# Performance work log

Measured on AMD Instinct MI355X. Metric: run time of the kernel, lower is better.

The kernel has to match this reference:

```python
import jax, jax.numpy as jnp
import numpy as np

N_NODES = 50000
N_EDGES = 800000
IN_CH = 256
HID = 64
OUT_CH = 64
N_LAYERS = 3
ALPHA = 0.1


def _gpr_temp():
    t = ALPHA * (1.0 - ALPHA) ** np.arange(N_LAYERS + 1)
    t[-1] = (1.0 - ALPHA) ** N_LAYERS
    return jnp.asarray(t, dtype=jnp.float32)


def setup_inputs() -> dict:
    key = jax.random.key(0)
    ks = jax.random.split(key, 8)
    x = jax.random.normal(ks[0], (N_NODES, IN_CH), dtype=jnp.float32)
    edge_index = jax.random.randint(ks[1], (2, N_EDGES), 0, N_NODES, dtype=jnp.int64 if jax.config.jax_enable_x64 else jnp.int32).astype(jnp.int32)
    edge_w = jax.random.uniform(ks[2], (N_EDGES,), dtype=jnp.float32)
    # xavier-uniform-ish scales
    W_in = jax.random.normal(ks[3], (IN_CH, HID), dtype=jnp.float32) * (1.0 / np.sqrt(IN_CH))
    b_in = jnp.zeros((HID,), dtype=jnp.float32)
    layer_W = jax.random.normal(ks[4], (N_LAYERS, HID, HID), dtype=jnp.float32) * (1.0 / np.sqrt(HID))
    layer_b = jnp.zeros((N_LAYERS, HID), dtype=jnp.float32)
    W_out = jax.random.normal(ks[5], (HID, OUT_CH), dtype=jnp.float32) * (1.0 / np.sqrt(HID))
    b_out = jnp.zeros((OUT_CH,), dtype=jnp.float32)
    temp = _gpr_temp()
    return {"x": x, "edge_index": edge_index, "edge_w": edge_w, "W_in": W_in,
            "b_in": b_in, "layer_W": layer_W, "layer_b": layer_b,
            "W_out": W_out, "b_out": b_out, "temp": temp}


def reference(x, edge_index, edge_w, W_in, b_in, layer_W, layer_b, W_out, b_out, temp):
    src, dst = edge_index[0], edge_index[1]
    # inlinear
    h = x @ W_in + b_in                      # [N, HID]
    # GPR combination: hidden = sum_k temp[k] * relu(SpMM(linear(h_k)))
    hidden = h * temp[0]
    cur = h
    for i in range(layer_W.shape[0]):
        z = cur @ layer_W[i] + layer_b[i]    # [N, HID]
        m = z[src] * edge_w[:, None]         # gather + edge weight, [E, HID]
        agg = jax.ops.segment_sum(m, dst, num_segments=x.shape[0])  # scatter-sum
        cur = jax.nn.relu(agg)               # dropout is identity in eval mode
        hidden = hidden + cur * temp[i + 1]
    return hidden @ W_out + b_out            # [N, OUT_CH]
```

## Files before the change

### kernel.cpp

```cpp
#include <hip/hip_runtime.h>
#include <hip/hip_bf16.h>

#define NN 50000
#define NE 800000
#define CIN 256
#define HH 64
#define NBINS 196
#define B1 256
#define EPB 3125
#define NGB 782
#define NLB 3125

typedef unsigned long long u64;
typedef __attribute__((ext_vector_type(8))) short short8;
typedef __attribute__((ext_vector_type(4))) float f32x4;

__device__ __forceinline__ float bf2f(ushort u) {
    union { unsigned int i; float f; } v; v.i = ((unsigned int)u) << 16; return v.f;
}
__device__ __forceinline__ ushort f2bf(float f) {
    __hip_bfloat16 b = __float2bfloat16(f);
    return *reinterpret_cast<ushort*>(&b);
}

__global__ __launch_bounds__(256) void k_prep(
    const float* __restrict__ W_in, const float* __restrict__ LW,
    const float* __restrict__ W_out, ushort* __restrict__ Wp)
{
    const int tid = blockIdx.x * 256 + threadIdx.x;
    if (tid < 16384) {
        const int i = tid & 7;
        const int l = (tid >> 3) & 63;
        const int s = (tid >> 9) & 7;
        const int t = tid >> 12;
        const int k = s * 32 + (l >> 4) * 8 + i;
        const int c = t * 16 + (l & 15);
        Wp[tid] = f2bf(W_in[k * HH + c]);
    } else {
        const int q = (tid - 16384) & 4095;
        const int m = (tid - 16384) >> 12;
        const int i = q & 7;
        const int l = (q >> 3) & 63;
        const int s = (q >> 9) & 1;
        const int t = q >> 10;
        const int k = s * 32 + (l >> 4) * 8 + i;
        const int c = t * 16 + (l & 15);
        const float* Wm = (m < 3) ? (LW + m * HH * HH) : W_out;
        Wp[tid] = f2bf(Wm[k * HH + c]);
    }
}

__global__ __launch_bounds__(256) void k_fused(
    const float* __restrict__ x, const ushort* __restrict__ Wp,
    const float* __restrict__ b, const int* __restrict__ dst,
    int* __restrict__ H, ushort* __restrict__ h_bf)
{
    __shared__ int hist[NBINS];
    if (blockIdx.x < B1) {
        for (int t = threadIdx.x; t < NBINS; t += 256) hist[t] = 0;
        __syncthreads();
        const int e0 = blockIdx.x * EPB;
        for (int i = threadIdx.x; i < EPB; i += 256)
            atomicAdd(&hist[dst[e0 + i] >> 8], 1);
        __syncthreads();
        for (int t = threadIdx.x; t < NBINS; t += 256)
            H[t * B1 + blockIdx.x] = hist[t];
        return;
    }
    const int w = threadIdx.x >> 6;
    const int l = threadIdx.x & 63;
    const int R0 = (blockIdx.x - B1) * 64 + w * 16;
    const int arow = R0 + (l & 15);
    const int xrow = (arow < NN) ? arow : (NN - 1);
    const float* xr = x + (size_t)xrow * CIN + (l >> 4) * 8;
    const short8* WpV = (const short8*)Wp;

    f32x4 acc0 = {0,0,0,0}, acc1 = {0,0,0,0}, acc2 = {0,0,0,0}, acc3 = {0,0,0,0};
    #pragma unroll
    for (int s = 0; s < 8; ++s) {
        const float4 xa = *(const float4*)(xr + s * 32);
        const float4 xb = *(const float4*)(xr + s * 32 + 4);
        short8 af;
        af[0] = (short)f2bf(xa.x); af[1] = (short)f2bf(xa.y);
        af[2] = (short)f2bf(xa.z); af[3] = (short)f2bf(xa.w);
        af[4] = (short)f2bf(xb.x); af[5] = (short)f2bf(xb.y);
        af[6] = (short)f2bf(xb.z); af[7] = (short)f2bf(xb.w);
        acc0 = __builtin_amdgcn_mfma_f32_16x16x32_bf16(af, WpV[(0*8+s)*64 + l], acc0, 0, 0, 0);
        acc1 = __builtin_amdgcn_mfma_f32_16x16x32_bf16(af, WpV[(1*8+s)*64 + l], acc1, 0, 0, 0);
        acc2 = __builtin_amdgcn_mfma_f32_16x16x32_bf16(af, WpV[(2*8+s)*64 + l], acc2, 0, 0, 0);
        acc3 = __builtin_amdgcn_mfma_f32_16x16x32_bf16(af, WpV[(3*8+s)*64 + l], acc3, 0, 0, 0);
    }
    const int colb = l & 15;
    const int rbase = R0 + (l >> 4) * 4;
    #pragma unroll
    for (int t = 0; t < 4; ++t) {
        const f32x4 a = (t == 0) ? acc0 : (t == 1) ? acc1 : (t == 2) ? acc2 : acc3;
        const float bb = b[t * 16 + colb];
        #pragma unroll
        for (int r = 0; r < 4; ++r) {
            const int row = rbase + r;
            if (row < NN)
                h_bf[(size_t)row * HH + t * 16 + colb] = f2bf(a[r] + bb);
        }
    }
}

__global__ __launch_bounds__(256) void k_scan(
    int* __restrict__ H, int* __restrict__ Sx, int* __restrict__ bcnt)
{
    __shared__ int s[256];
    const int b = blockIdx.x;
    const int t = threadIdx.x;
    int partial = 0;
    for (int idx = t; idx < b * B1; idx += 256) partial += H[idx];
    s[t] = partial;
    __syncthreads();
    #pragma unroll
    for (int off = 128; off > 0; off >>= 1) {
        if (t < off) s[t] += s[t + off];
        __syncthreads();
    }
    const int base = s[0];
    __syncthreads();
    const int v = H[b * B1 + t];
    s[t] = v;
    __syncthreads();
    #pragma unroll
    for (int off = 1; off < 256; off <<= 1) {
        const int add = (t >= off) ? s[t - off] : 0;
        __syncthreads();
        s[t] += add;
        __syncthreads();
    }
    H[b * B1 + t] = s[t] - v + base;
    if (t == 255) { Sx[b] = base; bcnt[b] = s[255]; }
}

__global__ __launch_bounds__(256) void k_scatterA(
    const int* __restrict__ src, const int* __restrict__ dst,
    const float* __restrict__ ew, const int* __restrict__ H,
    int2* __restrict__ tmp_e, ushort* __restrict__ tmp_low)
{
    __shared__ int cur[NBINS];
    for (int t = threadIdx.x; t < NBINS; t += 256)
        cur[t] = H[t * B1 + blockIdx.x];
    __syncthreads();
    const int e0 = blockIdx.x * EPB;
    for (int i = threadIdx.x; i < EPB; i += 256) {
        const int e = e0 + i;
        const int d = dst[e];
        const int pos = atomicAdd(&cur[d >> 8], 1);
        tmp_e[pos] = make_int2(src[e], __float_as_int(ew[e]));
        tmp_low[pos] = (ushort)(d & 255);
    }
}

__global__ __launch_bounds__(512) void k_sortB(
    const int2* __restrict__ tmp_e, const ushort* __restrict__ tmp_low,
    const int* __restrict__ Sx, const int* __restrict__ bcnt,
    int2* __restrict__ epack, int* __restrict__ rowptr, int* __restrict__ cnt)
{
    __shared__ int hist[256], s[256], curs[256];
    const int b = blockIdx.x;
    const int base = Sx[b];
    const int cntE = bcnt[b];
    const int t = threadIdx.x;
    if (t < 256) hist[t] = 0;
    __syncthreads();
    for (int i = t; i < cntE; i += 512)
        atomicAdd(&hist[tmp_low[base + i]], 1);
    __syncthreads();
    if (t < 256) s[t] = hist[t];
    __syncthreads();
    #pragma unroll
    for (int off = 1; off < 256; off <<= 1) {
        const int add = (t < 256 && t >= off) ? s[t - off] : 0;
        __syncthreads();
        if (t < 256) s[t] += add;
        __syncthreads();
    }
    if (t < 256) {
        const int excl = s[t] - hist[t];
        curs[t] = excl;
        const int d = b * 256 + t;
        if (d < NN) { rowptr[d] = base + excl; cnt[d] = hist[t]; }
    }
    __syncthreads();
    for (int i = t; i < cntE; i += 512) {
        const int2 e = tmp_e[base + i];
        const int low = (int)tmp_low[base + i];
        const int pos = base + atomicAdd(&curs[low], 1);
        epack[pos] = e;
    }
}

template<bool FINAL>
__global__ __launch_bounds__(256) void k_layer(
    const ushort* __restrict__ cur_in, ushort* __restrict__ cur_out,
    const int2* __restrict__ epack, const int* __restrict__ rowptr,
    const int* __restrict__ cnt,
    const ushort* __restrict__ WpL, const float* __restrict__ bvec,
    const float* __restrict__ temp,
    const ushort* __restrict__ hbf, const ushort* __restrict__ c1,
    const ushort* __restrict__ WpO, const float* __restrict__ bout,
    float* __restrict__ outp)
{
    __shared__ int2  es[4][64];
    __shared__ ushort ts[16][72];
    __shared__ float swv[16];
    const int w = threadIdx.x >> 6;
    const int j = threadIdx.x & 63;
    const int nb = blockIdx.x * 16;
    const int cg  = j >> 4;
    const int ch4 = j & 15;

    int rsA[4], rcA[4];
    #pragma unroll
    for (int q = 0; q < 4; ++q) {
        rsA[q] = rowptr[nb + w * 4 + q];
        rcA[q] = cnt[nb + w * 4 + q];
    }
    int2 pf = epack[min(rsA[0] + ((j < rcA[0]) ? j : 0), NE - 1)];

    #pragma unroll
    for (int q = 0; q < 4; ++q) {
        const int rs = rsA[q];
        const int rc = rcA[q];
        es[w][j] = pf;
        if (q < 3)
            pf = epack[min(rsA[q+1] + ((j < rcA[q+1]) ? j : 0), NE - 1)];

        float4 acc = {0.0f, 0.0f, 0.0f, 0.0f};
        float  sw  = 0.0f;
        const int m0 = min(rc, 64);
        for (int g = 0; g < m0; g += 16) {
            #pragma unroll
            for (int u = 0; u < 4; ++u) {
                const int idx = g + u * 4 + cg;
                const int sel = (idx < m0) ? idx : 0;
                const int2 p = es[w][sel];
                const float wgt = (idx < m0) ? __int_as_float(p.y) : 0.0f;
                const uint2 v = *(const uint2*)(cur_in + (size_t)p.x * HH + ch4 * 4);
                acc.x = fmaf(wgt, bf2f((ushort)(v.x & 0xffff)), acc.x);
                acc.y = fmaf(wgt, bf2f((ushort)(v.x >> 16)),    acc.y);
                acc.z = fmaf(wgt, bf2f((ushort)(v.y & 0xffff)), acc.z);
                acc.w = fmaf(wgt, bf2f((ushort)(v.y >> 16)),    acc.w);
                sw += wgt;
            }
        }
        for (int base = 64; base < rc; base += 64) {
            const int m = min(rc - base, 64);
            if (j < m) es[w][j] = epack[rs + base + j];
            for (int g = 0; g < m; g += 16) {
                #pragma unroll
                for (int u = 0; u < 4; ++u) {
                    const int idx = g + u * 4 + cg;
                    const int sel = (idx < m) ? idx : 0;
                    const int2 p = es[w][sel];
                    const float wgt = (idx < m) ? __int_as_float(p.y) : 0.0f;
                    const uint2 v = *(const uint2*)(cur_in + (size_t)p.x * HH + ch4 * 4);
                    acc.x = fmaf(wgt, bf2f((ushort)(v.x & 0xffff)), acc.x);
                    acc.y = fmaf(wgt, bf2f((ushort)(v.x >> 16)),    acc.y);
                    acc.z = fmaf(wgt, bf2f((ushort)(v.y & 0xffff)), acc.z);
                    acc.w = fmaf(wgt, bf2f((ushort)(v.y >> 16)),    acc.w);
                    sw += wgt;
                }
            }
        }
        #pragma unroll
        for (int off = 16; off < 64; off <<= 1) {
            acc.x += __shfl_xor(acc.x, off);
            acc.y += __shfl_xor(acc.y, off);
            acc.z += __shfl_xor(acc.z, off);
            acc.w += __shfl_xor(acc.w, off);
            sw    += __shfl_xor(sw, off);
        }
        if (j < 16) {
            const int node = w * 4 + q;
            uint2 o;
            o.x = (uint)f2bf(acc.x) | ((uint)f2bf(acc.y) << 16);
            o.y = (uint)f2bf(acc.z) | ((uint)f2bf(acc.w) << 16);
            *(uint2*)&ts[node][ch4 * 4] = o;
            if (j == 0) swv[node] = sw;
        }
    }
    __syncthreads();

    const int lr = j & 15;
    const int lg = j >> 4;
    const short8 a0 = *(const short8*)&ts[lr][lg * 8];
    const short8 a1 = *(const short8*)&ts[lr][32 + lg * 8];
    if (FINAL) __syncthreads();

    const short8* WpV = (const short8*)WpL;
    f32x4 zac = {0,0,0,0};
    zac = __builtin_amdgcn_mfma_f32_16x16x32_bf16(a0, WpV[(w*2+0)*64 + j], zac, 0, 0, 0);
    zac = __builtin_amdgcn_mfma_f32_16x16x32_bf16(a1, WpV[(w*2+1)*64 + j], zac, 0, 0, 0);

    const float bb = bvec[w * 16 + lr];
    float t0v = 0, t1v = 0, t2v = 0, t3v = 0;
    if (FINAL) { t0v = temp[0]; t1v = temp[1]; t2v = temp[2]; t3v = temp[3]; }
    #pragma unroll
    for (int r = 0; r < 4; ++r) {
        const int row = lg * 4 + r;
        const int n   = nb + row;
        const float z = zac[r] + swv[row] * bb;
        const float rv = fmaxf(z, 0.0f);
        const size_t o = (size_t)n * HH + w * 16 + lr;
        if (!FINAL) {
            cur_out[o] = f2bf(rv);
        } else {
            const float hid = t0v * bf2f(hbf[o]) + t1v * bf2f(c1[o])
                            + t2v * bf2f(cur_in[o]) + t3v * rv;
            ts[row][w * 16 + lr] = f2bf(hid);
        }
    }
    if (FINAL) {
        __syncthreads();
        const short8 b0 = *(const short8*)&ts[lr][lg * 8];
        const short8 b1 = *(const short8*)&ts[lr][32 + lg * 8];
        const short8* WoV = (const short8*)WpO;
        f32x4 oz = {0,0,0,0};
        oz = __builtin_amdgcn_mfma_f32_16x16x32_bf16(b0, WoV[(w*2+0)*64 + j], oz, 0, 0, 0);
        oz = __builtin_amdgcn_mfma_f32_16x16x32_bf16(b1, WoV[(w*2+1)*64 + j], oz, 0, 0, 0);
        const float bo = bout[w * 16 + lr];
        #pragma unroll
        for (int r = 0; r < 4; ++r) {
            const int row = lg * 4 + r;
            outp[(size_t)(nb + row) * HH + w * 16 + lr] = oz[r] + bo;
        }
    }
}

extern "C" void kernel_launch(void* const* d_in, const int* in_sizes, int n_in,
                              void* d_out, int out_size, void* d_ws, size_t ws_size,
                              hipStream_t stream)
{
    const float* x     = (const float*)d_in[0];
    const int*   ei    = (const int*)d_in[1];
    const float* ew    = (const float*)d_in[2];
    const float* W_in  = (const float*)d_in[3];
    const float* b_in  = (const float*)d_in[4];
    const float* LW    = (const float*)d_in[5];
    const float* Lb    = (const float*)d_in[6];
    const float* W_out = (const float*)d_in[7];
    const float* b_out = (const float*)d_in[8];
    const float* temp  = (const float*)d_in[9];
    const int* src = ei;
    const int* dst = ei + NE;

    char* p = (char*)d_ws;
    ushort* h_bf    = (ushort*)p;  p += (size_t)NN * HH * 2;
    ushort* curA    = (ushort*)p;  p += (size_t)NN * HH * 2;
    ushort* curB    = (ushort*)p;  p += (size_t)NN * HH * 2;
    int2*   epack   = (int2*)p;    p += (size_t)NE * 8;
    int2*   tmp_e   = (int2*)p;    p += (size_t)NE * 8;
    ushort* tmp_low = (ushort*)p;  p += (size_t)NE * 2;
    int*    H       = (int*)p;     p += (size_t)NBINS * B1 * 4;
    int*    Sx      = (int*)p;     p += (NBINS + 1) * 4;
    int*    bcnt    = (int*)p;     p += NBINS * 4;
    int*    rowptr  = (int*)p;     p += (size_t)NN * 4;
    int*    cnt     = (int*)p;     p += (size_t)NN * 4;
    ushort* Wp      = (ushort*)p;  p += 32768 * 2;
    float*  out     = (float*)d_out;

    const ushort* WpIn  = Wp;
    const ushort* WpL0  = Wp + 16384;
    const ushort* WpL1  = Wp + 16384 + 4096;
    const ushort* WpL2  = Wp + 16384 + 2 * 4096;
    const ushort* WpOut = Wp + 16384 + 3 * 4096;

    k_prep<<<128, 256, 0, stream>>>(W_in, LW, W_out, Wp);
    k_fused<<<B1 + NGB, 256, 0, stream>>>(x, WpIn, b_in, dst, H, h_bf);
    k_scan<<<NBINS, 256, 0, stream>>>(H, Sx, bcnt);
    k_scatterA<<<B1, 256, 0, stream>>>(src, dst, ew, H, tmp_e, tmp_low);
    k_sortB<<<NBINS, 512, 0, stream>>>(tmp_e, tmp_low, Sx, bcnt, epack, rowptr, cnt);

    k_layer<false><<<NLB, 256, 0, stream>>>(h_bf, curA, epack, rowptr, cnt,
                                            WpL0, Lb + 0 * HH, temp,
                                            nullptr, nullptr, nullptr, nullptr, nullptr);
    k_layer<false><<<NLB, 256, 0, stream>>>(curA, curB, epack, rowptr, cnt,
                                            WpL1, Lb + 1 * HH, temp,
                                            nullptr, nullptr, nullptr, nullptr, nullptr);
    k_layer<true><<<NLB, 256, 0, stream>>>(curB, nullptr, epack, rowptr, cnt,
                                           WpL2, Lb + 2 * HH, temp,
                                           h_bf, curA, WpOut, b_out, out);
}
```

Before: 134.7 us.

## Reorder CSR build stages, pack low dst bits into src, fuse scatter with GEMM

Moves the per-block destination histogram into the weight-prep kernel, runs the scan next, then fuses the first-pass bucket scatter with the input GEMM kernel, cutting one launch. The low 8 bits of dst are packed into the upper half of the src word, which removes the separate tmp_low array and its reads and writes. The GEMM path also preloads all x vectors into registers before the MFMA loop. The packing assumes src fits in 16 bits; node indices up to 49999 do fit, and the high-byte mask in sortB recovers it.

After: 127.4 us (median of 2 runs). 1.06x faster.

```diff
diff --git a/kernel.cpp b/kernel.cpp
--- a/kernel.cpp
+++ b/kernel.cpp
@@ -23,11 +23,24 @@
     return *reinterpret_cast<ushort*>(&b);
 }
 
-__global__ __launch_bounds__(256) void k_prep(
+__global__ __launch_bounds__(256) void k_prep_hist(
     const float* __restrict__ W_in, const float* __restrict__ LW,
-    const float* __restrict__ W_out, ushort* __restrict__ Wp)
-{
-    const int tid = blockIdx.x * 256 + threadIdx.x;
+    const float* __restrict__ W_out, ushort* __restrict__ Wp,
+    const int* __restrict__ dst, int* __restrict__ H)
+{
+    __shared__ int hist[NBINS];
+    if (blockIdx.x < B1) {
+        for (int t = threadIdx.x; t < NBINS; t += 256) hist[t] = 0;
+        __syncthreads();
+        const int e0 = blockIdx.x * EPB;
+        for (int i = threadIdx.x; i < EPB; i += 256)
+            atomicAdd(&hist[dst[e0 + i] >> 8], 1);
+        __syncthreads();
+        for (int t = threadIdx.x; t < NBINS; t += 256)
+            H[t * B1 + blockIdx.x] = hist[t];
+        return;
+    }
+    const int tid = (blockIdx.x - B1) * 256 + threadIdx.x;
     if (tid < 16384) {
         const int i = tid & 7;
         const int l = (tid >> 3) & 63;
@@ -50,21 +63,56 @@
     }
 }
 
-__global__ __launch_bounds__(256) void k_fused(
+__global__ __launch_bounds__(256) void k_scan(
+    int* __restrict__ H, int* __restrict__ Sx, int* __restrict__ bcnt)
+{
+    __shared__ int s[256];
+    const int b = blockIdx.x;
+    const int t = threadIdx.x;
+    int partial = 0;
+    for (int idx = t; idx < b * B1; idx += 256) partial += H[idx];
+    s[t] = partial;
+    __syncthreads();
+    #pragma unroll
+    for (int off = 128; off > 0; off >>= 1) {
+        if (t < off) s[t] += s[t + off];
+        __syncthreads();
+    }
+    const int base = s[0];
+    __syncthreads();
+    const int v = H[b * B1 + t];
+    s[t] = v;
+    __syncthreads();
+    #pragma unroll
+    for (int off = 1; off < 256; off <<= 1) {
+        const int add = (t >= off) ? s[t - off] : 0;
+        __syncthreads();
+        s[t] += add;
+        __syncthreads();
+    }
+    H[b * B1 + t] = s[t] - v + base;
+    if (t == 255) { Sx[b] = base; bcnt[b] = s[255]; }
+}
+
+__global__ __launch_bounds__(256) void k_fused2(
     const float* __restrict__ x, const ushort* __restrict__ Wp,
-    const float* __restrict__ b, const int* __restrict__ dst,
-    int* __restrict__ H, ushort* __restrict__ h_bf)
-{
-    __shared__ int hist[NBINS];
+    const float* __restrict__ b,
+    const int* __restrict__ src, const int* __restrict__ dst,
+    const float* __restrict__ ew, const int* __restrict__ H,
+    int2* __restrict__ tmp_e, ushort* __restrict__ h_bf)
+{
+    __shared__ int cur[NBINS];
     if (blockIdx.x < B1) {
-        for (int t = threadIdx.x; t < NBINS; t += 256) hist[t] = 0;
+        for (int t = threadIdx.x; t < NBINS; t += 256)
+            cur[t] = H[t * B1 + blockIdx.x];
         __syncthreads();
         const int e0 = blockIdx.x * EPB;
-        for (int i = threadIdx.x; i < EPB; i += 256)
-            atomicAdd(&hist[dst[e0 + i] >> 8], 1);
-        __syncthreads();
-        for (int t = threadIdx.x; t < NBINS; t += 256)
-            H[t * B1 + blockIdx.x] = hist[t];
+        for (int i = threadIdx.x; i < EPB; i += 256) {
+            const int e = e0 + i;
+            const int d = dst[e];
+            const int pos = atomicAdd(&cur[d >> 8], 1);
+            tmp_e[pos] = make_int2(src[e] | ((d & 255) << 16), __float_as_int(ew[e]));
+        }
         return;
     }
     const int w = threadIdx.x >> 6;
@@ -73,13 +121,20 @@
     const int arow = R0 + (l & 15);
     const int xrow = (arow < NN) ? arow : (NN - 1);
     const float* xr = x + (size_t)xrow * CIN + (l >> 4) * 8;
+
+    float4 xv[16];
+    #pragma unroll
+    for (int s = 0; s < 8; ++s) {
+        xv[2*s]   = *(const float4*)(xr + s * 32);
+        xv[2*s+1] = *(const float4*)(xr + s * 32 + 4);
+    }
+
     const short8* WpV = (const short8*)Wp;
-
     f32x4 acc0 = {0,0,0,0}, acc1 = {0,0,0,0}, acc2 = {0,0,0,0}, acc3 = {0,0,0,0};
     #pragma unroll
     for (int s = 0; s < 8; ++s) {
-        const float4 xa = *(const float4*)(xr + s * 32);
-        const float4 xb = *(const float4*)(xr + s * 32 + 4);
+        const float4 xa = xv[2*s];
+        const float4 xb = xv[2*s+1];
         short8 af;
         af[0] = (short)f2bf(xa.x); af[1] = (short)f2bf(xa.y);
         af[2] = (short)f2bf(xa.z); af[3] = (short)f2bf(xa.w);
@@ -105,58 +160,8 @@
     }
 }
 
-__global__ __launch_bounds__(256) void k_scan(
-    int* __restrict__ H, int* __restrict__ Sx, int* __restrict__ bcnt)
-{
-    __shared__ int s[256];
-    const int b = blockIdx.x;
-    const int t = threadIdx.x;
-    int partial = 0;
-    for (int idx = t; idx < b * B1; idx += 256) partial += H[idx];
-    s[t] = partial;
-    __syncthreads();
-    #pragma unroll
-    for (int off = 128; off > 0; off >>= 1) {
-        if (t < off) s[t] += s[t + off];
-        __syncthreads();
-    }
-    const int base = s[0];
-    __syncthreads();
-    const int v = H[b * B1 + t];
-    s[t] = v;
-    __syncthreads();
-    #pragma unroll
-    for (int off = 1; off < 256; off <<= 1) {
-        const int add = (t >= off) ? s[t - off] : 0;
-        __syncthreads();
-        s[t] += add;
-        __syncthreads();
-    }
-    H[b * B1 + t] = s[t] - v + base;
-    if (t == 255) { Sx[b] = base; bcnt[b] = s[255]; }
-}
-
-__global__ __launch_bounds__(256) void k_scatterA(
-    const int* __restrict__ src, const int* __restrict__ dst,
-    const float* __restrict__ ew, const int* __restrict__ H,
-    int2* __restrict__ tmp_e, ushort* __restrict__ tmp_low)
-{
-    __shared__ int cur[NBINS];
-    for (int t = threadIdx.x; t < NBINS; t += 256)
-        cur[t] = H[t * B1 + blockIdx.x];
-    __syncthreads();
-    const int e0 = blockIdx.x * EPB;
-    for (int i = threadIdx.x; i < EPB; i += 256) {
-        const int e = e0 + i;
-        const int d = dst[e];
-        const int pos = atomicAdd(&cur[d >> 8], 1);
-        tmp_e[pos] = make_int2(src[e], __float_as_int(ew[e]));
-        tmp_low[pos] = (ushort)(d & 255);
-    }
-}
-
 __global__ __launch_bounds__(512) void k_sortB(
-    const int2* __restrict__ tmp_e, const ushort* __restrict__ tmp_low,
+    const int2* __restrict__ tmp_e,
     const int* __restrict__ Sx, const int* __restrict__ bcnt,
     int2* __restrict__ epack, int* __restrict__ rowptr, int* __restrict__ cnt)
 {
@@ -168,7 +173,7 @@
     if (t < 256) hist[t] = 0;
     __syncthreads();
     for (int i = t; i < cntE; i += 512)
-        atomicAdd(&hist[tmp_low[base + i]], 1);
+        atomicAdd(&hist[(tmp_e[base + i].x >> 16) & 255], 1);
     __syncthreads();
     if (t < 256) s[t] = hist[t];
     __syncthreads();
@@ -188,9 +193,9 @@
     __syncthreads();
     for (int i = t; i < cntE; i += 512) {
         const int2 e = tmp_e[base + i];
-        const int low = (int)tmp_low[base + i];
+        const int low = (e.x >> 16) & 255;
         const int pos = base + atomicAdd(&curs[low], 1);
-        epack[pos] = e;
+        epack[pos] = make_int2(e.x & 0xFFFF, e.y);
     }
 }
 
@@ -355,7 +360,6 @@
     ushort* curB    = (ushort*)p;  p += (size_t)NN * HH * 2;
     int2*   epack   = (int2*)p;    p += (size_t)NE * 8;
     int2*   tmp_e   = (int2*)p;    p += (size_t)NE * 8;
-    ushort* tmp_low = (ushort*)p;  p += (size_t)NE * 2;
     int*    H       = (int*)p;     p += (size_t)NBINS * B1 * 4;
     int*    Sx      = (int*)p;     p += (NBINS + 1) * 4;
     int*    bcnt    = (int*)p;     p += NBINS * 4;
@@ -370,11 +374,11 @@
     const ushort* WpL2  = Wp + 16384 + 2 * 4096;
     const ushort* WpOut = Wp + 16384 + 3 * 4096;
 
-    k_prep<<<128, 256, 0, stream>>>(W_in, LW, W_out, Wp);
-    k_fused<<<B1 + NGB, 256, 0, stream>>>(x, WpIn, b_in, dst, H, h_bf);
+    k_prep_hist<<<B1 + 128, 256, 0, stream>>>(W_in, LW, W_out, Wp, dst, H);
     k_scan<<<NBINS, 256, 0, stream>>>(H, Sx, bcnt);
-    k_scatterA<<<B1, 256, 0, stream>>>(src, dst, ew, H, tmp_e, tmp_low);
-    k_sortB<<<NBINS, 512, 0, stream>>>(tmp_e, tmp_low, Sx, bcnt, epack, rowptr, cnt);
+    k_fused2<<<B1 + NGB, 256, 0, stream>>>(x, WpIn, b_in, src, dst, ew, H,
+                                           tmp_e, h_bf);
+    k_sortB<<<NBINS, 512, 0, stream>>>(tmp_e, Sx, bcnt, epack, rowptr, cnt);
 
     k_layer<false><<<NLB, 256, 0, stream>>>(h_bf, curA, epack, rowptr, cnt,
                                             WpL0, Lb + 0 * HH, temp,
```
